# Performance work log

Measured on AMD Instinct MI355X. Metric: run time of the kernel, lower is better.

Reference implementation:

```python
import jax, jax.numpy as jnp
import numpy as np

COORD = 5.0   # self.coord
NOOBJ = 0.5   # self.noobj
B = 32768
S = 7.0       # grid size, hard-coded as /7 in the original


def setup_inputs() -> dict:
    key = jax.random.key(0)
    k1, k2, k3 = jax.random.split(key, 3)
    # min 0.01 keeps sqrt(wh) and its gradient finite (original takes sqrt of raw preds)
    output = jax.random.uniform(k1, (B, 7, 7, 30), dtype=jnp.float32, minval=0.01, maxval=1.0)
    target = jax.random.uniform(k2, (B, 7, 7, 30), dtype=jnp.float32, minval=0.01, maxval=1.0)
    obj = (jax.random.uniform(k3, (B, 7, 7)) < 0.15).astype(jnp.float32)
    target = target.at[..., 4].set(obj).at[..., 9].set(obj)
    return {"output": output, "target": target}


def reference(output, target):
    dt = output.dtype
    w_obj = (target[..., 4] > 0).astype(dt)      # (B,7,7) object-cell mask
    w_no = 1.0 - w_obj                            # no-object cells

    out_b = output[..., :10].reshape(output.shape[0], 7, 7, 2, 5)
    tgt_b = target[..., :10].reshape(target.shape[0], 7, 7, 2, 5)
    out_cls = output[..., 10:]
    tgt_cls = target[..., 10:]

    # class MSE (sum) over object cells
    class_loss = jnp.sum(w_obj[..., None] * (out_cls - tgt_cls) ** 2)
    accurate_num = jnp.sum(w_obj * (jnp.argmax(out_cls, -1) == jnp.argmax(tgt_cls, -1)).astype(dt))

    # box corners: xy/7 -+ 0.5*wh (as in the original)
    o_xy, o_wh = out_b[..., :2] / S, out_b[..., 2:4]
    o_lt, o_rb = o_xy - 0.5 * o_wh, o_xy + 0.5 * o_wh          # (B,7,7,2,2)
    t_box = tgt_b[..., 0, :]                                    # target box 0 (as in loop: target_boxes[i])
    t_xy, t_wh = t_box[..., :2] / S, t_box[..., 2:4]
    t_lt = (t_xy - 0.5 * t_wh)[..., None, :]                    # (B,7,7,1,2)
    t_rb = (t_xy + 0.5 * t_wh)[..., None, :]

    # torchvision.ops.box_iou: inter / (area1 + area2 - inter), widths clamped at 0
    inter_wh = jnp.clip(jnp.minimum(o_rb, t_rb) - jnp.maximum(o_lt, t_lt), 0.0)
    inter = inter_wh[..., 0] * inter_wh[..., 1]                 # (B,7,7,2)
    area_o = (o_rb - o_lt)[..., 0] * (o_rb - o_lt)[..., 1]
    area_t = (t_rb - t_lt)[..., 0] * (t_rb - t_lt)[..., 1]
    iou = inter / (area_o + area_t - inter)                     # (B,7,7,2)

    resp = jnp.argmax(iou, -1)                                  # responsible box index
    max_iou = jnp.max(iou, -1)
    left = jax.nn.one_hot(resp, 2, dtype=dt)                    # (B,7,7,2)

    out_sel = jnp.sum(left[..., None] * out_b, axis=-2)         # responsible predicted box
    tgt_sel = jnp.sum(left[..., None] * tgt_b, axis=-2)         # target box at same slot
    out_ab = jnp.sum((1.0 - left)[..., None] * out_b, axis=-2)  # abandoned predicted box

    coord_loss = jnp.sum(w_obj * (
        jnp.sum((out_sel[..., :2] - tgt_sel[..., :2]) ** 2, -1)
        + jnp.sum((jnp.sqrt(out_sel[..., 2:4]) - jnp.sqrt(tgt_sel[..., 2:4])) ** 2, -1)))
    conf_loss = jnp.sum(w_obj * (out_sel[..., 4] - max_iou) ** 2)
    abandon_loss = jnp.sum(w_obj * out_ab[..., 4] ** 2)         # box_iou target is 0 at abandoned slot
    noobj_loss = jnp.sum(w_no[..., None] * (out_b[..., 4] - tgt_b[..., 4]) ** 2)

    total = COORD * coord_loss + conf_loss + NOOBJ * (noobj_loss + abandon_loss) + class_loss
    sum_iou = jnp.sum(w_obj * max_iou)
    return total, sum_iou, accurate_num
```

## Files before the change

kernel.cpp:

```cpp
#include <hip/hip_runtime.h>
#include <stdint.h>

#define S_INV (1.0f / 7.0f)
#define COORD_W 5.0f
#define NOOBJ_W 0.5f

#define SLICE_FLOATS 3840
#define WAVES_PER_BLOCK 4

typedef const __attribute__((address_space(1))) void* gp1_t;
typedef __attribute__((address_space(3))) void* lp3_t;

__global__ __launch_bounds__(256) void yolo_loss_kernel(
    const float* __restrict__ outp, const float* __restrict__ tgtp,
    float* __restrict__ ws, int nchunks, int nwaves)
{
    __shared__ float lds[WAVES_PER_BLOCK * SLICE_FLOATS];

    const int wave = threadIdx.x >> 6;
    const int lane = threadIdx.x & 63;
    const int gwave = blockIdx.x * WAVES_PER_BLOCK + wave;

    float* slice = lds + wave * SLICE_FLOATS;

    float acc_total = 0.f, acc_iou = 0.f, acc_acc = 0.f;

    for (int m = gwave; m < nchunks; m += nwaves) {
        const size_t cbase = (size_t)m * (64 * 120);

#pragma unroll
        for (int j = 0; j < 15; ++j) {
            const int off = j * 1024 + lane * 16;
            const char* src = (off < 7680)
                ? (const char*)outp + cbase + off
                : (const char*)tgtp + cbase + (off - 7680);
            __builtin_amdgcn_global_load_lds((gp1_t)src,
                                             (lp3_t)(slice + j * 256),
                                             16, 0, 0);
        }
        asm volatile("s_waitcnt vmcnt(0)" ::: "memory");
        __builtin_amdgcn_sched_barrier(0);

        const float* oc = slice + lane * 30;
        const float* tc = slice + 1920 + lane * 30;
        float ov[30], tv[30];
#pragma unroll
        for (int i = 0; i < 15; ++i) {
            float2 a = *reinterpret_cast<const float2*>(oc + 2 * i);
            float2 b = *reinterpret_cast<const float2*>(tc + 2 * i);
            ov[2 * i] = a.x; ov[2 * i + 1] = a.y;
            tv[2 * i] = b.x; tv[2 * i + 1] = b.y;
        }

        float w_obj = (tv[4] > 0.f) ? 1.f : 0.f;
        float w_no = 1.f - w_obj;

        float cls = 0.f;
        float omax = ov[10]; int oarg = 0;
        float tmax = tv[10]; int targ = 0;
#pragma unroll
        for (int c = 0; c < 20; ++c) {
            float d = ov[10 + c] - tv[10 + c];
            cls += d * d;
            if (ov[10 + c] > omax) { omax = ov[10 + c]; oarg = c; }
            if (tv[10 + c] > tmax) { tmax = tv[10 + c]; targ = c; }
        }

        float t_x = tv[0] * S_INV, t_y = tv[1] * S_INV;
        float t_w = tv[2], t_h = tv[3];
        float t_l = t_x - 0.5f * t_w, t_r = t_x + 0.5f * t_w;
        float t_t = t_y - 0.5f * t_h, t_b = t_y + 0.5f * t_h;
        float area_t = t_w * t_h;

        float iou0, iou1;
        {
            float x = ov[0] * S_INV, y = ov[1] * S_INV;
            float w = ov[2], h = ov[3];
            float l = x - 0.5f * w, r = x + 0.5f * w;
            float tt = y - 0.5f * h, bb = y + 0.5f * h;
            float iw = fmaxf(fminf(r, t_r) - fmaxf(l, t_l), 0.f);
            float ih = fmaxf(fminf(bb, t_b) - fmaxf(tt, t_t), 0.f);
            float inter = iw * ih;
            iou0 = inter / (w * h + area_t - inter);
        }
        {
            float x = ov[5] * S_INV, y = ov[6] * S_INV;
            float w = ov[7], h = ov[8];
            float l = x - 0.5f * w, r = x + 0.5f * w;
            float tt = y - 0.5f * h, bb = y + 0.5f * h;
            float iw = fmaxf(fminf(r, t_r) - fmaxf(l, t_l), 0.f);
            float ih = fmaxf(fminf(bb, t_b) - fmaxf(tt, t_t), 0.f);
            float inter = iw * ih;
            iou1 = inter / (w * h + area_t - inter);
        }

        bool r1 = (iou1 > iou0);
        float max_iou = r1 ? iou1 : iou0;

        float os0 = r1 ? ov[5] : ov[0];
        float os1 = r1 ? ov[6] : ov[1];
        float os2 = r1 ? ov[7] : ov[2];
        float os3 = r1 ? ov[8] : ov[3];
        float os4 = r1 ? ov[9] : ov[4];
        float ts0 = r1 ? tv[5] : tv[0];
        float ts1 = r1 ? tv[6] : tv[1];
        float ts2 = r1 ? tv[7] : tv[2];
        float ts3 = r1 ? tv[8] : tv[3];
        float oa4 = r1 ? ov[4] : ov[9];

        float d0 = os0 - ts0, d1 = os1 - ts1;
        float d2 = sqrtf(os2) - sqrtf(ts2);
        float d3 = sqrtf(os3) - sqrtf(ts3);
        float coord = d0 * d0 + d1 * d1 + d2 * d2 + d3 * d3;

        float dc = os4 - max_iou;
        float conf = dc * dc;
        float aband = oa4 * oa4;
        float n0 = ov[4] - tv[4], n1 = ov[9] - tv[9];
        float noobj = n0 * n0 + n1 * n1;

        float cell_total = w_obj * (COORD_W * coord + conf + NOOBJ_W * aband + cls)
                         + NOOBJ_W * w_no * noobj;

        acc_total += cell_total;
        acc_iou   += w_obj * max_iou;
        acc_acc   += w_obj * ((oarg == targ) ? 1.f : 0.f);

        __builtin_amdgcn_sched_barrier(0);
    }

#pragma unroll
    for (int off = 32; off > 0; off >>= 1) {
        acc_total += __shfl_down(acc_total, off);
        acc_iou   += __shfl_down(acc_iou, off);
        acc_acc   += __shfl_down(acc_acc, off);
    }
    if (lane == 0) {
        ws[gwave]              = acc_total;
        ws[nwaves + gwave]     = acc_iou;
        ws[2 * nwaves + gwave] = acc_acc;
    }
}

__global__ __launch_bounds__(256) void yolo_reduce_kernel(
    const float* __restrict__ ws, float* __restrict__ out, int nwaves)
{
    float t0 = 0.f, t1 = 0.f, t2 = 0.f;
    for (int i = threadIdx.x; i < nwaves; i += blockDim.x) {
        t0 += ws[i];
        t1 += ws[nwaves + i];
        t2 += ws[2 * nwaves + i];
    }
#pragma unroll
    for (int off = 32; off > 0; off >>= 1) {
        t0 += __shfl_down(t0, off);
        t1 += __shfl_down(t1, off);
        t2 += __shfl_down(t2, off);
    }
    __shared__ float s[3][4];
    int wave = threadIdx.x >> 6;
    int lane = threadIdx.x & 63;
    if (lane == 0) { s[0][wave] = t0; s[1][wave] = t1; s[2][wave] = t2; }
    __syncthreads();
    if (threadIdx.x == 0) {
        float a0 = 0.f, a1 = 0.f, a2 = 0.f;
#pragma unroll
        for (int w = 0; w < 4; ++w) { a0 += s[0][w]; a1 += s[1][w]; a2 += s[2][w]; }
        out[0] = a0;
        out[1] = a1;
        out[2] = a2;
    }
}

extern "C" void kernel_launch(void* const* d_in, const int* in_sizes, int n_in,
                              void* d_out, int out_size, void* d_ws, size_t ws_size,
                              hipStream_t stream) {
    const float* outp = (const float*)d_in[0];
    const float* tgtp = (const float*)d_in[1];
    float* ws = (float*)d_ws;
    float* o = (float*)d_out;

    const int ncells  = in_sizes[0] / 30;
    const int nchunks = ncells / 64;
    const int blocks  = 2048;
    const int nwaves  = blocks * WAVES_PER_BLOCK;

    yolo_loss_kernel<<<blocks, 256, 0, stream>>>(outp, tgtp, ws, nchunks, nwaves);
    yolo_reduce_kernel<<<1, 256, 0, stream>>>(ws, o, nwaves);
}
```

Baseline: 79.33 us.

## Double-buffer per-wave LDS staging and shrink grid to 256 blocks

Each wave now keeps two LDS slices. It issues the global-to-LDS loads for its next chunk before computing the current one, and waits with vmcnt(15) so only the current chunk's loads must have landed. The grid drops from 2048 to 256 blocks, so each wave handles more chunks and the prefetch has more iterations to overlap with. The trade-off is double the LDS per block (about 120KB), which limits resident blocks per CU, and far fewer waves in flight to hide memory latency.

Result: faster. 73.55 us (median of 2 runs) (-7.3%).

```diff
diff --git a/kernel.cpp b/kernel.cpp
--- a/kernel.cpp
+++ b/kernel.cpp
@@ -10,39 +10,56 @@
 
 typedef const __attribute__((address_space(1))) void* gp1_t;
 typedef __attribute__((address_space(3))) void* lp3_t;
+
+__device__ __forceinline__ void stage_chunk(const float* __restrict__ outp,
+                                            const float* __restrict__ tgtp,
+                                            float* dst, int m, int lane)
+{
+    const size_t cb = (size_t)m * (64 * 120);
+#pragma unroll
+    for (int j = 0; j < 15; ++j) {
+        const int off = j * 1024 + lane * 16;
+        const char* src = (off < 7680)
+            ? (const char*)outp + cb + off
+            : (const char*)tgtp + cb + (off - 7680);
+        __builtin_amdgcn_global_load_lds((gp1_t)src, (lp3_t)(dst + j * 256),
+                                         16, 0, 0);
+    }
+}
 
 __global__ __launch_bounds__(256) void yolo_loss_kernel(
     const float* __restrict__ outp, const float* __restrict__ tgtp,
     float* __restrict__ ws, int nchunks, int nwaves)
 {
-    __shared__ float lds[WAVES_PER_BLOCK * SLICE_FLOATS];
+    __shared__ float lds[WAVES_PER_BLOCK * 2 * SLICE_FLOATS];
 
     const int wave = threadIdx.x >> 6;
     const int lane = threadIdx.x & 63;
     const int gwave = blockIdx.x * WAVES_PER_BLOCK + wave;
 
-    float* slice = lds + wave * SLICE_FLOATS;
+    float* bufA = lds + wave * 2 * SLICE_FLOATS;
+    float* bufB = bufA + SLICE_FLOATS;
 
     float acc_total = 0.f, acc_iou = 0.f, acc_acc = 0.f;
 
+    if (gwave < nchunks) stage_chunk(outp, tgtp, bufA, gwave, lane);
+    int cur = 0;
+
     for (int m = gwave; m < nchunks; m += nwaves) {
-        const size_t cbase = (size_t)m * (64 * 120);
-
-#pragma unroll
-        for (int j = 0; j < 15; ++j) {
-            const int off = j * 1024 + lane * 16;
-            const char* src = (off < 7680)
-                ? (const char*)outp + cbase + off
-                : (const char*)tgtp + cbase + (off - 7680);
-            __builtin_amdgcn_global_load_lds((gp1_t)src,
-                                             (lp3_t)(slice + j * 256),
-                                             16, 0, 0);
-        }
-        asm volatile("s_waitcnt vmcnt(0)" ::: "memory");
+        const bool has_next = (m + nwaves) < nchunks;
+        float* bnext = cur ? bufA : bufB;
+        float* bcur  = cur ? bufB : bufA;
+
+        if (has_next) {
+            stage_chunk(outp, tgtp, bnext, m + nwaves, lane);
+            asm volatile("s_waitcnt vmcnt(15)" ::: "memory");
+        } else {
+            asm volatile("s_waitcnt vmcnt(0)" ::: "memory");
+        }
         __builtin_amdgcn_sched_barrier(0);
 
-        const float* oc = slice + lane * 30;
-        const float* tc = slice + 1920 + lane * 30;
+        const float* oc = bcur + lane * 30;
+        const float* tc = bcur + 1920 + lane * 30;
         float ov[30], tv[30];
 #pragma unroll
         for (int i = 0; i < 15; ++i) {
@@ -127,6 +144,7 @@
         acc_acc   += w_obj * ((oarg == targ) ? 1.f : 0.f);
 
         __builtin_amdgcn_sched_barrier(0);
+        cur ^= 1;
     }
 
 #pragma unroll
@@ -182,7 +200,7 @@
 
     const int ncells  = in_sizes[0] / 30;
     const int nchunks = ncells / 64;
-    const int blocks  = 2048;
+    const int blocks  = 256;
     const int nwaves  = blocks * WAVES_PER_BLOCK;
 
     yolo_loss_kernel<<<blocks, 256, 0, stream>>>(outp, tgtp, ws, nchunks, nwaves);
```

## Assign contiguous cell ranges per wave and register-prefetch next chunk

Applied to the files above, without the earlier changes.

Replaces the strided grid loop with async global-to-LDS loads by a persistent layout. Each of 2048 waves (256 blocks of 512 threads) now owns a contiguous range of cells. The next 64-cell chunk is loaded into registers while the current chunk is computed, then written into the wave's LDS slice, overlapping memory latency with ALU work. A per-lane tail path handles the leftover cells. The aim is better streaming locality and latency hiding for this bandwidth-bound loss. The cost is more register pressure from the prefetch buffer and fewer total waves in flight.

Measured after the change: 163.3 us. +105.9%, slower.

```diff
diff --git a/kernel.cpp b/kernel.cpp
--- a/kernel.cpp
+++ b/kernel.cpp
@@ -5,15 +5,91 @@
 #define COORD_W 5.0f
 #define NOOBJ_W 0.5f
 
+#define WAVES_PER_BLOCK 8
 #define SLICE_FLOATS 3840
-#define WAVES_PER_BLOCK 4
-
-typedef const __attribute__((address_space(1))) void* gp1_t;
-typedef __attribute__((address_space(3))) void* lp3_t;
-
-__global__ __launch_bounds__(256) void yolo_loss_kernel(
+#define CHUNK_CELLS 64
+#define CHUNK_BYTES (CHUNK_CELLS * 120)
+
+__device__ __forceinline__ void cell_loss(const float* ov, const float* tv,
+                                          float& acc_total, float& acc_iou,
+                                          float& acc_acc)
+{
+    float w_obj = (tv[4] > 0.f) ? 1.f : 0.f;
+    float w_no = 1.f - w_obj;
+
+    float cls = 0.f;
+    float omax = ov[10]; int oarg = 0;
+    float tmax = tv[10]; int targ = 0;
+#pragma unroll
+    for (int c = 0; c < 20; ++c) {
+        float d = ov[10 + c] - tv[10 + c];
+        cls += d * d;
+        if (ov[10 + c] > omax) { omax = ov[10 + c]; oarg = c; }
+        if (tv[10 + c] > tmax) { tmax = tv[10 + c]; targ = c; }
+    }
+
+    float t_x = tv[0] * S_INV, t_y = tv[1] * S_INV;
+    float t_w = tv[2], t_h = tv[3];
+    float t_l = t_x - 0.5f * t_w, t_r = t_x + 0.5f * t_w;
+    float t_t = t_y - 0.5f * t_h, t_b = t_y + 0.5f * t_h;
+    float area_t = t_w * t_h;
+
+    float iou0, iou1;
+    {
+        float x = ov[0] * S_INV, y = ov[1] * S_INV;
+        float w = ov[2], h = ov[3];
+        float l = x - 0.5f * w, r = x + 0.5f * w;
+        float tt = y - 0.5f * h, bb = y + 0.5f * h;
+        float iw = fmaxf(fminf(r, t_r) - fmaxf(l, t_l), 0.f);
+        float ih = fmaxf(fminf(bb, t_b) - fmaxf(tt, t_t), 0.f);
+        float inter = iw * ih;
+        iou0 = inter / (w * h + area_t - inter);
+    }
+    {
+        float x = ov[5] * S_INV, y = ov[6] * S_INV;
+        float w = ov[7], h = ov[8];
+        float l = x - 0.5f * w, r = x + 0.5f * w;
+        float tt = y - 0.5f * h, bb = y + 0.5f * h;
+        float iw = fmaxf(fminf(r, t_r) - fmaxf(l, t_l), 0.f);
+        float ih = fmaxf(fminf(bb, t_b) - fmaxf(tt, t_t), 0.f);
+        float inter = iw * ih;
+        iou1 = inter / (w * h + area_t - inter);
+    }
+
+    bool r1 = (iou1 > iou0);
+    float max_iou = r1 ? iou1 : iou0;
+
+    float os0 = r1 ? ov[5] : ov[0];
+    float os1 = r1 ? ov[6] : ov[1];
+    float os2 = r1 ? ov[7] : ov[2];
+    float os3 = r1 ? ov[8] : ov[3];
+    float os4 = r1 ? ov[9] : ov[4];
+    float ts0 = r1 ? tv[5] : tv[0];
+    float ts1 = r1 ? tv[6] : tv[1];
+    float ts2 = r1 ? tv[7] : tv[2];
+    float ts3 = r1 ? tv[8] : tv[3];
+    float oa4 = r1 ? ov[4] : ov[9];
+
+    float d0 = os0 - ts0, d1 = os1 - ts1;
+    float d2 = sqrtf(os2) - sqrtf(ts2);
+    float d3 = sqrtf(os3) - sqrtf(ts3);
+    float coord = d0 * d0 + d1 * d1 + d2 * d2 + d3 * d3;
+
+    float dc = os4 - max_iou;
+    float conf = dc * dc;
+    float aband = oa4 * oa4;
+    float n0 = ov[4] - tv[4], n1 = ov[9] - tv[9];
+    float noobj = n0 * n0 + n1 * n1;
+
+    acc_total += w_obj * (COORD_W * coord + conf + NOOBJ_W * aband + cls)
+               + NOOBJ_W * w_no * noobj;
+    acc_iou   += w_obj * max_iou;
+    acc_acc   += w_obj * ((oarg == targ) ? 1.f : 0.f);
+}
+
+__global__ __launch_bounds__(512) void yolo_loss_kernel(
     const float* __restrict__ outp, const float* __restrict__ tgtp,
-    float* __restrict__ ws, int nchunks, int nwaves)
+    float* __restrict__ ws, int cells_per_wave, int nwaves)
 {
     __shared__ float lds[WAVES_PER_BLOCK * SLICE_FLOATS];
 
@@ -22,28 +98,45 @@
     const int gwave = blockIdx.x * WAVES_PER_BLOCK + wave;
 
     float* slice = lds + wave * SLICE_FLOATS;
+    const size_t wbase = (size_t)gwave * cells_per_wave * 120;
+
+    const int nmain = cells_per_wave / CHUNK_CELLS;
+    const int ntail = cells_per_wave - nmain * CHUNK_CELLS;
 
     float acc_total = 0.f, acc_iou = 0.f, acc_acc = 0.f;
 
-    for (int m = gwave; m < nchunks; m += nwaves) {
-        const size_t cbase = (size_t)m * (64 * 120);
-
-#pragma unroll
-        for (int j = 0; j < 15; ++j) {
-            const int off = j * 1024 + lane * 16;
-            const char* src = (off < 7680)
-                ? (const char*)outp + cbase + off
-                : (const char*)tgtp + cbase + (off - 7680);
-            __builtin_amdgcn_global_load_lds((gp1_t)src,
-                                             (lp3_t)(slice + j * 256),
-                                             16, 0, 0);
-        }
-        asm volatile("s_waitcnt vmcnt(0)" ::: "memory");
-        __builtin_amdgcn_sched_barrier(0);
+    float4 pre[15];
+#pragma unroll
+    for (int j = 0; j < 15; ++j) {
+        const int off = j * 1024 + lane * 16;
+        const char* src = (off < 7680)
+            ? (const char*)outp + wbase + off
+            : (const char*)tgtp + wbase + (off - 7680);
+        pre[j] = *reinterpret_cast<const float4*>(src);
+    }
+#pragma unroll
+    for (int j = 0; j < 15; ++j)
+        *reinterpret_cast<float4*>((char*)slice + j * 1024 + lane * 16) = pre[j];
+
+    float ov[30], tv[30];
+
+#pragma unroll 1
+    for (int c = 0; c < nmain; ++c) {
+        const bool has_next = (c + 1) < nmain;
+        if (has_next) {
+            const size_t cb = wbase + (size_t)(c + 1) * CHUNK_BYTES;
+#pragma unroll
+            for (int j = 0; j < 15; ++j) {
+                const int off = j * 1024 + lane * 16;
+                const char* src = (off < 7680)
+                    ? (const char*)outp + cb + off
+                    : (const char*)tgtp + cb + (off - 7680);
+                pre[j] = *reinterpret_cast<const float4*>(src);
+            }
+        }
 
         const float* oc = slice + lane * 30;
         const float* tc = slice + 1920 + lane * 30;
-        float ov[30], tv[30];
 #pragma unroll
         for (int i = 0; i < 15; ++i) {
             float2 a = *reinterpret_cast<const float2*>(oc + 2 * i);
@@ -52,81 +145,28 @@
             tv[2 * i] = b.x; tv[2 * i + 1] = b.y;
         }
 
-        float w_obj = (tv[4] > 0.f) ? 1.f : 0.f;
-        float w_no = 1.f - w_obj;
-
-        float cls = 0.f;
-        float omax = ov[10]; int oarg = 0;
-        float tmax = tv[10]; int targ = 0;
-#pragma unroll
-        for (int c = 0; c < 20; ++c) {
-            float d = ov[10 + c] - tv[10 + c];
-            cls += d * d;
-            if (ov[10 + c] > omax) { omax = ov[10 + c]; oarg = c; }
-            if (tv[10 + c] > tmax) { tmax = tv[10 + c]; targ = c; }
-        }
-
-        float t_x = tv[0] * S_INV, t_y = tv[1] * S_INV;
-        float t_w = tv[2], t_h = tv[3];
-        float t_l = t_x - 0.5f * t_w, t_r = t_x + 0.5f * t_w;
-        float t_t = t_y - 0.5f * t_h, t_b = t_y + 0.5f * t_h;
-        float area_t = t_w * t_h;
-
-        float iou0, iou1;
-        {
-            float x = ov[0] * S_INV, y = ov[1] * S_INV;
-            float w = ov[2], h = ov[3];
-            float l = x - 0.5f * w, r = x + 0.5f * w;
-            float tt = y - 0.5f * h, bb = y + 0.5f * h;
-            float iw = fmaxf(fminf(r, t_r) - fmaxf(l, t_l), 0.f);
-            float ih = fmaxf(fminf(bb, t_b) - fmaxf(tt, t_t), 0.f);
-            float inter = iw * ih;
-            iou0 = inter / (w * h + area_t - inter);
-        }
-        {
-            float x = ov[5] * S_INV, y = ov[6] * S_INV;
-            float w = ov[7], h = ov[8];
-            float l = x - 0.5f * w, r = x + 0.5f * w;
-            float tt = y - 0.5f * h, bb = y + 0.5f * h;
-            float iw = fmaxf(fminf(r, t_r) - fmaxf(l, t_l), 0.f);
-            float ih = fmaxf(fminf(bb, t_b) - fmaxf(tt, t_t), 0.f);
-            float inter = iw * ih;
-            iou1 = inter / (w * h + area_t - inter);
-        }
-
-        bool r1 = (iou1 > iou0);
-        float max_iou = r1 ? iou1 : iou0;
-
-        float os0 = r1 ? ov[5] : ov[0];
-        float os1 = r1 ? ov[6] : ov[1];
-        float os2 = r1 ? ov[7] : ov[2];
-        float os3 = r1 ? ov[8] : ov[3];
-        float os4 = r1 ? ov[9] : ov[4];
-        float ts0 = r1 ? tv[5] : tv[0];
-        float ts1 = r1 ? tv[6] : tv[1];
-        float ts2 = r1 ? tv[7] : tv[2];
-        float ts3 = r1 ? tv[8] : tv[3];
-        float oa4 = r1 ? ov[4] : ov[9];
-
-        float d0 = os0 - ts0, d1 = os1 - ts1;
-        float d2 = sqrtf(os2) - sqrtf(ts2);
-        float d3 = sqrtf(os3) - sqrtf(ts3);
-        float coord = d0 * d0 + d1 * d1 + d2 * d2 + d3 * d3;
-
-        float dc = os4 - max_iou;
-        float conf = dc * dc;
-        float aband = oa4 * oa4;
-        float n0 = ov[4] - tv[4], n1 = ov[9] - tv[9];
-        float noobj = n0 * n0 + n1 * n1;
-
-        float cell_total = w_obj * (COORD_W * coord + conf + NOOBJ_W * aband + cls)
-                         + NOOBJ_W * w_no * noobj;
-
-        acc_total += cell_total;
-        acc_iou   += w_obj * max_iou;
-        acc_acc   += w_obj * ((oarg == targ) ? 1.f : 0.f);
-
         __builtin_amdgcn_sched_barrier(0);
+
+        cell_loss(ov, tv, acc_total, acc_iou, acc_acc);
+
+        if (has_next) {
+#pragma unroll
+            for (int j = 0; j < 15; ++j)
+                *reinterpret_cast<float4*>((char*)slice + j * 1024 + lane * 16) = pre[j];
+        }
+    }
+
+    if (lane < ntail) {
+        const char* oc = (const char*)outp + wbase + (size_t)(nmain * CHUNK_CELLS + lane) * 120;
+        const char* tc = (const char*)tgtp + wbase + (size_t)(nmain * CHUNK_CELLS + lane) * 120;
+#pragma unroll
+        for (int i = 0; i < 15; ++i) {
+            float2 a = *reinterpret_cast<const float2*>(oc + 8 * i);
+            float2 b = *reinterpret_cast<const float2*>(tc + 8 * i);
+            ov[2 * i] = a.x; ov[2 * i + 1] = a.y;
+            tv[2 * i] = b.x; tv[2 * i + 1] = b.y;
+        }
+        cell_loss(ov, tv, acc_total, acc_iou, acc_acc);
     }
 
 #pragma unroll
@@ -180,11 +220,11 @@
     float* ws = (float*)d_ws;
     float* o = (float*)d_out;
 
-    const int ncells  = in_sizes[0] / 30;
-    const int nchunks = ncells / 64;
-    const int blocks  = 2048;
-    const int nwaves  = blocks * WAVES_PER_BLOCK;
-
-    yolo_loss_kernel<<<blocks, 256, 0, stream>>>(outp, tgtp, ws, nchunks, nwaves);
+    const int ncells = in_sizes[0] / 30;
+    const int blocks = 256;
+    const int nwaves = blocks * WAVES_PER_BLOCK;
+    const int cells_per_wave = ncells / nwaves;
+
+    yolo_loss_kernel<<<blocks, 512, 0, stream>>>(outp, tgtp, ws, cells_per_wave, nwaves);
     yolo_reduce_kernel<<<1, 256, 0, stream>>>(ws, o, nwaves);
 }
```

## Replace LDS-staged wave loads with direct per-thread float4 loads of cell pairs

Applied to the files above, without the earlier changes.

Drops the global_load_lds staging through shared memory. Each thread now loads two adjacent cells (60 floats, 15 float4) straight from global memory into registers and computes both cells' losses. The grid shrinks from 2048 to 256 blocks. This removes LDS traffic and the explicit waitcnt/sched barriers. The cost is per-thread strided float4 accesses (240-byte stride across lanes), which coalesce poorly, plus higher register pressure and fewer waves to hide memory latency.

New measurement: 142.9 us. 1.8x slower.

```diff
diff --git a/kernel.cpp b/kernel.cpp
--- a/kernel.cpp
+++ b/kernel.cpp
@@ -5,128 +5,113 @@
 #define COORD_W 5.0f
 #define NOOBJ_W 0.5f
 
-#define SLICE_FLOATS 3840
-#define WAVES_PER_BLOCK 4
 
-typedef const __attribute__((address_space(1))) void* gp1_t;
-typedef __attribute__((address_space(3))) void* lp3_t;
+__device__ __forceinline__ void cell_loss(const float* ov, const float* tv,
+                                          float& acc_total, float& acc_iou,
+                                          float& acc_acc)
+{
+    float w_obj = (tv[4] > 0.f) ? 1.f : 0.f;
+    float w_no = 1.f - w_obj;
 
-__global__ __launch_bounds__(256) void yolo_loss_kernel(
+    float cls = 0.f;
+    float omax = ov[10]; int oarg = 0;
+    float tmax = tv[10]; int targ = 0;
+#pragma unroll
+    for (int c = 0; c < 20; ++c) {
+        float d = ov[10 + c] - tv[10 + c];
+        cls += d * d;
+        if (ov[10 + c] > omax) { omax = ov[10 + c]; oarg = c; }
+        if (tv[10 + c] > tmax) { tmax = tv[10 + c]; targ = c; }
+    }
+
+    float t_x = tv[0] * S_INV, t_y = tv[1] * S_INV;
+    float t_w = tv[2], t_h = tv[3];
+    float t_l = t_x - 0.5f * t_w, t_r = t_x + 0.5f * t_w;
+    float t_t = t_y - 0.5f * t_h, t_b = t_y + 0.5f * t_h;
+    float area_t = t_w * t_h;
+
+    float iou0, iou1;
+    {
+        float x = ov[0] * S_INV, y = ov[1] * S_INV;
+        float w = ov[2], h = ov[3];
+        float l = x - 0.5f * w, r = x + 0.5f * w;
+        float tt = y - 0.5f * h, bb = y + 0.5f * h;
+        float iw = fmaxf(fminf(r, t_r) - fmaxf(l, t_l), 0.f);
+        float ih = fmaxf(fminf(bb, t_b) - fmaxf(tt, t_t), 0.f);
+        float inter = iw * ih;
+        iou0 = inter / (w * h + area_t - inter);
+    }
+    {
+        float x = ov[5] * S_INV, y = ov[6] * S_INV;
+        float w = ov[7], h = ov[8];
+        float l = x - 0.5f * w, r = x + 0.5f * w;
+        float tt = y - 0.5f * h, bb = y + 0.5f * h;
+        float iw = fmaxf(fminf(r, t_r) - fmaxf(l, t_l), 0.f);
+        float ih = fmaxf(fminf(bb, t_b) - fmaxf(tt, t_t), 0.f);
+        float inter = iw * ih;
+        iou1 = inter / (w * h + area_t - inter);
+    }
+
+    bool r1 = (iou1 > iou0);
+    float max_iou = r1 ? iou1 : iou0;
+
+    float os0 = r1 ? ov[5] : ov[0];
+    float os1 = r1 ? ov[6] : ov[1];
+    float os2 = r1 ? ov[7] : ov[2];
+    float os3 = r1 ? ov[8] : ov[3];
+    float os4 = r1 ? ov[9] : ov[4];
+    float ts0 = r1 ? tv[5] : tv[0];
+    float ts1 = r1 ? tv[6] : tv[1];
+    float ts2 = r1 ? tv[7] : tv[2];
+    float ts3 = r1 ? tv[8] : tv[3];
+    float oa4 = r1 ? ov[4] : ov[9];
+
+    float d0 = os0 - ts0, d1 = os1 - ts1;
+    float d2 = sqrtf(os2) - sqrtf(ts2);
+    float d3 = sqrtf(os3) - sqrtf(ts3);
+    float coord = d0 * d0 + d1 * d1 + d2 * d2 + d3 * d3;
+
+    float dc = os4 - max_iou;
+    float conf = dc * dc;
+    float aband = oa4 * oa4;
+    float n0 = ov[4] - tv[4], n1 = ov[9] - tv[9];
+    float noobj = n0 * n0 + n1 * n1;
+
+    acc_total += w_obj * (COORD_W * coord + conf + NOOBJ_W * aband + cls)
+               + NOOBJ_W * w_no * noobj;
+    acc_iou   += w_obj * max_iou;
+    acc_acc   += w_obj * ((oarg == targ) ? 1.f : 0.f);
+}
+
+__global__ void yolo_loss_kernel(
     const float* __restrict__ outp, const float* __restrict__ tgtp,
-    float* __restrict__ ws, int nchunks, int nwaves)
+    float* __restrict__ ws, int npairs, int nthreads)
 {
-    __shared__ float lds[WAVES_PER_BLOCK * SLICE_FLOATS];
-
-    const int wave = threadIdx.x >> 6;
-    const int lane = threadIdx.x & 63;
-    const int gwave = blockIdx.x * WAVES_PER_BLOCK + wave;
-
-    float* slice = lds + wave * SLICE_FLOATS;
+    const int g = blockIdx.x * blockDim.x + threadIdx.x;
 
     float acc_total = 0.f, acc_iou = 0.f, acc_acc = 0.f;
 
-    for (int m = gwave; m < nchunks; m += nwaves) {
-        const size_t cbase = (size_t)m * (64 * 120);
+    for (int p = g; p < npairs; p += nthreads) {
+        const float4* po = reinterpret_cast<const float4*>(outp) + (size_t)p * 15;
+        const float4* pt = reinterpret_cast<const float4*>(tgtp) + (size_t)p * 15;
 
+        float4 o4[15], t4[15];
+#pragma unroll
+        for (int j = 0; j < 15; ++j) o4[j] = po[j];
+#pragma unroll
+        for (int j = 0; j < 15; ++j) t4[j] = pt[j];
+
+        float od[60], td[60];
 #pragma unroll
         for (int j = 0; j < 15; ++j) {
-            const int off = j * 1024 + lane * 16;
-            const char* src = (off < 7680)
-                ? (const char*)outp + cbase + off
-                : (const char*)tgtp + cbase + (off - 7680);
-            __builtin_amdgcn_global_load_lds((gp1_t)src,
-                                             (lp3_t)(slice + j * 256),
-                                             16, 0, 0);
-        }
-        asm volatile("s_waitcnt vmcnt(0)" ::: "memory");
-        __builtin_amdgcn_sched_barrier(0);
-
-        const float* oc = slice + lane * 30;
-        const float* tc = slice + 1920 + lane * 30;
-        float ov[30], tv[30];
-#pragma unroll
-        for (int i = 0; i < 15; ++i) {
-            float2 a = *reinterpret_cast<const float2*>(oc + 2 * i);
-            float2 b = *reinterpret_cast<const float2*>(tc + 2 * i);
-            ov[2 * i] = a.x; ov[2 * i + 1] = a.y;
-            tv[2 * i] = b.x; tv[2 * i + 1] = b.y;
+            od[4 * j] = o4[j].x; od[4 * j + 1] = o4[j].y;
+            od[4 * j + 2] = o4[j].z; od[4 * j + 3] = o4[j].w;
+            td[4 * j] = t4[j].x; td[4 * j + 1] = t4[j].y;
+            td[4 * j + 2] = t4[j].z; td[4 * j + 3] = t4[j].w;
         }
 
-        float w_obj = (tv[4] > 0.f) ? 1.f : 0.f;
-        float w_no = 1.f - w_obj;
-
-        float cls = 0.f;
-        float omax = ov[10]; int oarg = 0;
-        float tmax = tv[10]; int targ = 0;
-#pragma unroll
-        for (int c = 0; c < 20; ++c) {
-            float d = ov[10 + c] - tv[10 + c];
-            cls += d * d;
-            if (ov[10 + c] > omax) { omax = ov[10 + c]; oarg = c; }
-            if (tv[10 + c] > tmax) { tmax = tv[10 + c]; targ = c; }
-        }
-
-        float t_x = tv[0] * S_INV, t_y = tv[1] * S_INV;
-        float t_w = tv[2], t_h = tv[3];
-        float t_l = t_x - 0.5f * t_w, t_r = t_x + 0.5f * t_w;
-        float t_t = t_y - 0.5f * t_h, t_b = t_y + 0.5f * t_h;
-        float area_t = t_w * t_h;
-
-        float iou0, iou1;
-        {
-            float x = ov[0] * S_INV, y = ov[1] * S_INV;
-            float w = ov[2], h = ov[3];
-            float l = x - 0.5f * w, r = x + 0.5f * w;
-            float tt = y - 0.5f * h, bb = y + 0.5f * h;
-            float iw = fmaxf(fminf(r, t_r) - fmaxf(l, t_l), 0.f);
-            float ih = fmaxf(fminf(bb, t_b) - fmaxf(tt, t_t), 0.f);
-            float inter = iw * ih;
-            iou0 = inter / (w * h + area_t - inter);
-        }
-        {
-            float x = ov[5] * S_INV, y = ov[6] * S_INV;
-            float w = ov[7], h = ov[8];
-            float l = x - 0.5f * w, r = x + 0.5f * w;
-            float tt = y - 0.5f * h, bb = y + 0.5f * h;
-            float iw = fmaxf(fminf(r, t_r) - fmaxf(l, t_l), 0.f);
-            float ih = fmaxf(fminf(bb, t_b) - fmaxf(tt, t_t), 0.f);
-            float inter = iw * ih;
-            iou1 = inter / (w * h + area_t - inter);
-        }
-
-        bool r1 = (iou1 > iou0);
-        float max_iou = r1 ? iou1 : iou0;
-
-        float os0 = r1 ? ov[5] : ov[0];
-        float os1 = r1 ? ov[6] : ov[1];
-        float os2 = r1 ? ov[7] : ov[2];
-        float os3 = r1 ? ov[8] : ov[3];
-        float os4 = r1 ? ov[9] : ov[4];
-        float ts0 = r1 ? tv[5] : tv[0];
-        float ts1 = r1 ? tv[6] : tv[1];
-        float ts2 = r1 ? tv[7] : tv[2];
-        float ts3 = r1 ? tv[8] : tv[3];
-        float oa4 = r1 ? ov[4] : ov[9];
-
-        float d0 = os0 - ts0, d1 = os1 - ts1;
-        float d2 = sqrtf(os2) - sqrtf(ts2);
-        float d3 = sqrtf(os3) - sqrtf(ts3);
-        float coord = d0 * d0 + d1 * d1 + d2 * d2 + d3 * d3;
-
-        float dc = os4 - max_iou;
-        float conf = dc * dc;
-        float aband = oa4 * oa4;
-        float n0 = ov[4] - tv[4], n1 = ov[9] - tv[9];
-        float noobj = n0 * n0 + n1 * n1;
-
-        float cell_total = w_obj * (COORD_W * coord + conf + NOOBJ_W * aband + cls)
-                         + NOOBJ_W * w_no * noobj;
-
-        acc_total += cell_total;
-        acc_iou   += w_obj * max_iou;
-        acc_acc   += w_obj * ((oarg == targ) ? 1.f : 0.f);
-
-        __builtin_amdgcn_sched_barrier(0);
+        cell_loss(od,      td,      acc_total, acc_iou, acc_acc);
+        cell_loss(od + 30, td + 30, acc_total, acc_iou, acc_acc);
     }
 
 #pragma unroll
@@ -135,10 +120,13 @@
         acc_iou   += __shfl_down(acc_iou, off);
         acc_acc   += __shfl_down(acc_acc, off);
     }
+    const int lane = threadIdx.x & 63;
+    const int gwid = g >> 6;
+    const int nwaves = nthreads >> 6;
     if (lane == 0) {
-        ws[gwave]              = acc_total;
-        ws[nwaves + gwave]     = acc_iou;
-        ws[2 * nwaves + gwave] = acc_acc;
+        ws[gwid]              = acc_total;
+        ws[nwaves + gwid]     = acc_iou;
+        ws[2 * nwaves + gwid] = acc_acc;
     }
 }
 
@@ -180,11 +168,13 @@
     float* ws = (float*)d_ws;
     float* o = (float*)d_out;
 
-    const int ncells  = in_sizes[0] / 30;
-    const int nchunks = ncells / 64;
-    const int blocks  = 2048;
-    const int nwaves  = blocks * WAVES_PER_BLOCK;
+    const int ncells   = in_sizes[0] / 30;
+    const int npairs   = ncells / 2;
+    const int blocks   = 256;
+    const int threads  = 256;
+    const int nthreads = blocks * threads;
+    const int nwaves   = nthreads / 64;
 
-    yolo_loss_kernel<<<blocks, 256, 0, stream>>>(outp, tgtp, ws, nchunks, nwaves);
+    yolo_loss_kernel<<<blocks, threads, 0, stream>>>(outp, tgtp, ws, npairs, nthreads);
     yolo_reduce_kernel<<<1, 256, 0, stream>>>(ws, o, nwaves);
 }
```
